# Optimization experiments

Measured on AMD Instinct MI355X. Metric: run time of the kernel, lower is better.

Reference implementation:

```python
import jax, jax.numpy as jnp
import numpy as np

N, H = 8192, 1024

def setup_inputs() -> dict:
    key = jax.random.key(0)
    ks = jax.random.split(key, 7)
    s = 1.0 / np.sqrt(H)
    return {
        "x": jax.random.normal(ks[0], (N, H), dtype=jnp.float32),
        "Wq": jax.random.uniform(ks[1], (H, H), dtype=jnp.float32, minval=-s, maxval=s),
        "bq": jax.random.uniform(ks[2], (H,), dtype=jnp.float32, minval=-s, maxval=s),
        "Wk": jax.random.uniform(ks[3], (H, H), dtype=jnp.float32, minval=-s, maxval=s),
        "bk": jax.random.uniform(ks[4], (H,), dtype=jnp.float32, minval=-s, maxval=s),
        "Wv": jax.random.uniform(ks[5], (H, H), dtype=jnp.float32, minval=-s, maxval=s),
        "bv": jax.random.uniform(ks[6], (H,), dtype=jnp.float32, minval=-s, maxval=s),
    }

def reference(x, Wq, bq, Wk, bk, Wv, bv):
    # q/k/v projections: [N, H]
    q = x @ Wq + bq
    k = x @ Wk + bk
    v = x @ Wv + bv
    # full scores [N, N]; NOTE: original has no 1/sqrt(d) scaling
    scores = q @ k.T
    alpha = jax.nn.softmax(scores, axis=1)
    return alpha @ v
```

## Files before the change

kernel.cpp:

```cpp
#include <hip/hip_runtime.h>
#include <hip/hip_bf16.h>
#include <hip/hip_fp16.h>


typedef _Float16 f16x8 __attribute__((ext_vector_type(8)));
typedef float floatx4 __attribute__((ext_vector_type(4)));

__device__ __forceinline__ unsigned short f2h(float f) {
  __half h = __float2half(f);
  return __builtin_bit_cast(unsigned short, h);
}

__device__ __forceinline__ void async16(const void* g, void* l) {
  __builtin_amdgcn_global_load_lds(
      (__attribute__((address_space(1))) unsigned int*)(g),
      (__attribute__((address_space(3))) unsigned int*)(l),
      16, 0, 0);
}


__global__ __launch_bounds__(256) void conv_f32_f16(const float* __restrict__ in,
                                                    unsigned short* __restrict__ out,
                                                    long n) {
  long i = ((long)blockIdx.x * 256 + threadIdx.x) * 4;
  if (i + 3 < n) {
    float4 f = *(const float4*)(in + i);
    ushort4 o;
    o.x = f2h(f.x); o.y = f2h(f.y); o.z = f2h(f.z); o.w = f2h(f.w);
    *(ushort4*)(out + i) = o;
  }
}

__global__ __launch_bounds__(256) void transpose_f32_f16(const float* __restrict__ in,
                                                         unsigned short* __restrict__ out,
                                                         int rows, int cols) {
  __shared__ float tile[32][33];
  int bx = blockIdx.x * 32;
  int by = blockIdx.y * 32;
  int tx = threadIdx.x & 31, ty = threadIdx.x >> 5;
  #pragma unroll
  for (int yy = ty; yy < 32; yy += 8)
    tile[yy][tx] = in[(size_t)(by + yy) * cols + bx + tx];
  __syncthreads();
  #pragma unroll
  for (int yy = ty; yy < 32; yy += 8)
    out[(size_t)(bx + yy) * rows + by + tx] = f2h(tile[tx][yy]);
}

__global__ __launch_bounds__(256) void transpose_u16(const unsigned short* __restrict__ in,
                                                     unsigned short* __restrict__ out,
                                                     int rows, int cols) {
  __shared__ unsigned short tile[32][33];
  int bx = blockIdx.x * 32;
  int by = blockIdx.y * 32;
  int tx = threadIdx.x & 31, ty = threadIdx.x >> 5;
  #pragma unroll
  for (int yy = ty; yy < 32; yy += 8)
    tile[yy][tx] = in[(size_t)(by + yy) * cols + bx + tx];
  __syncthreads();
  #pragma unroll
  for (int yy = ty; yy < 32; yy += 8)
    out[(size_t)(bx + yy) * rows + by + tx] = tile[tx][yy];
}

template <int MODE>
__global__ __launch_bounds__(256, 2)
void gemm_bt(const unsigned short* __restrict__ A,
             const unsigned short* __restrict__ B,
             int M, int Nn, int K,
             const float* __restrict__ bias,
             void* __restrict__ out) {
  __shared__ unsigned short As[128 * 32];
  __shared__ unsigned short Bs[128 * 32];
  const int tid  = threadIdx.x;
  const int wave = tid >> 6;
  const int lane = tid & 63;
  const int wm = wave >> 1, wn = wave & 1;
  const int quad = lane >> 4, l16 = lane & 15;
  const long bm = (long)blockIdx.y * 128;
  const long bn = (long)blockIdx.x * 128;

  floatx4 acc[4][4] = {};

  const int srow = wave * 32 + (lane >> 2);
  const int scol = (lane & 3) * 8;
  const unsigned short* gA0 = A + (bm + srow) * (long)K + scol;
  const unsigned short* gA1 = gA0 + 16L * K;
  const unsigned short* gB0 = B + (bn + srow) * (long)K + scol;
  const unsigned short* gB1 = gB0 + 16L * K;
  unsigned short* lA0 = &As[(wave * 32) * 32];
  unsigned short* lA1 = &As[(wave * 32 + 16) * 32];
  unsigned short* lB0 = &Bs[(wave * 32) * 32];
  unsigned short* lB1 = &Bs[(wave * 32 + 16) * 32];

  for (int kk = 0; kk < K; kk += 32) {
    async16(gA0 + kk, lA0);
    async16(gA1 + kk, lA1);
    async16(gB0 + kk, lB0);
    async16(gB1 + kk, lB1);
    __syncthreads();
    f16x8 af[4], bfv[4];
    #pragma unroll
    for (int i = 0; i < 4; ++i) {
      af[i]  = *reinterpret_cast<const f16x8*>(&As[(wm * 64 + i * 16 + l16) * 32 + quad * 8]);
      bfv[i] = *reinterpret_cast<const f16x8*>(&Bs[(wn * 64 + i * 16 + l16) * 32 + quad * 8]);
    }
    #pragma unroll
    for (int i = 0; i < 4; ++i)
      #pragma unroll
      for (int j = 0; j < 4; ++j)
        acc[i][j] = __builtin_amdgcn_mfma_f32_16x16x32_f16(af[i], bfv[j], acc[i][j], 0, 0, 0);
    __syncthreads();
  }

  #pragma unroll
  for (int i = 0; i < 4; ++i) {
    const long row0 = bm + wm * 64 + i * 16 + quad * 4;
    #pragma unroll
    for (int j = 0; j < 4; ++j) {
      const long col = bn + wn * 64 + j * 16 + l16;
      float badd = 0.0f;
      if constexpr (MODE == 0) badd = bias[col];
      #pragma unroll
      for (int r = 0; r < 4; ++r) {
        const float v = acc[i][j][r] + badd;
        const long idx = (row0 + r) * (long)Nn + col;
        if constexpr (MODE == 0) {
          ((unsigned short*)out)[idx] = f2h(v);
        } else if constexpr (MODE == 1) {
          ((unsigned short*)out)[idx] = f2h(v);
        } else {
          ((float*)out)[idx] = v;
        }
      }
    }
  }
}

__global__ __launch_bounds__(256) void softmax_rows(unsigned short* __restrict__ S, int n) {
  const int row = blockIdx.x;
  const int tid = threadIdx.x;
  const int lane = tid & 63, w = tid >> 6;
  unsigned short* prow = S + (size_t)row * n;
  const __half* hrow = (const __half*)prow;

  float v[32];
  float m = -1e30f;
  #pragma unroll
  for (int i = 0; i < 32; ++i) {
    v[i] = __half2float(hrow[i * 256 + tid]);
    m = fmaxf(m, v[i]);
  }
  #pragma unroll
  for (int off = 32; off > 0; off >>= 1) m = fmaxf(m, __shfl_down(m, off, 64));
  __shared__ float redm[4];
  if (lane == 0) redm[w] = m;
  __syncthreads();
  m = fmaxf(fmaxf(redm[0], redm[1]), fmaxf(redm[2], redm[3]));

  float s = 0.0f;
  #pragma unroll
  for (int i = 0; i < 32; ++i) {
    v[i] = __expf(v[i] - m);
    s += v[i];
  }
  #pragma unroll
  for (int off = 32; off > 0; off >>= 1) s += __shfl_down(s, off, 64);
  __shared__ float reds[4];
  if (lane == 0) reds[w] = s;
  __syncthreads();
  s = reds[0] + reds[1] + reds[2] + reds[3];
  const float inv = 1.0f / s;

  #pragma unroll
  for (int i = 0; i < 32; ++i) prow[i * 256 + tid] = f2h(v[i] * inv);
}

extern "C" void kernel_launch(void* const* d_in, const int* in_sizes, int n_in,
                              void* d_out, int out_size, void* d_ws, size_t ws_size,
                              hipStream_t stream) {
  const int N = 8192, H = 1024;
  const float* x  = (const float*)d_in[0];
  const float* Wq = (const float*)d_in[1];
  const float* bq = (const float*)d_in[2];
  const float* Wk = (const float*)d_in[3];
  const float* bk = (const float*)d_in[4];
  const float* Wv = (const float*)d_in[5];
  const float* bv = (const float*)d_in[6];

  char* p = (char*)d_ws;
  unsigned short* xh  = (unsigned short*)p; p += (size_t)N * H * 2;
  unsigned short* WqT = (unsigned short*)p; p += (size_t)H * H * 2;
  unsigned short* WkT = (unsigned short*)p; p += (size_t)H * H * 2;
  unsigned short* WvT = (unsigned short*)p; p += (size_t)H * H * 2;
  unsigned short* qh  = (unsigned short*)p; p += (size_t)N * H * 2;
  unsigned short* kh  = (unsigned short*)p; p += (size_t)N * H * 2;
  unsigned short* vh  = (unsigned short*)p; p += (size_t)N * H * 2;
  unsigned short* vth = (unsigned short*)p; p += (size_t)N * H * 2;
  unsigned short* S   = (unsigned short*)p; p += (size_t)N * N * 2;
  if ((size_t)(p - (char*)d_ws) > ws_size) return;

  conv_f32_f16<<<(N * H / 4 + 255) / 256, 256, 0, stream>>>(x, xh, (long)N * H);
  transpose_f32_f16<<<dim3(H / 32, H / 32), 256, 0, stream>>>(Wq, WqT, H, H);
  transpose_f32_f16<<<dim3(H / 32, H / 32), 256, 0, stream>>>(Wk, WkT, H, H);
  transpose_f32_f16<<<dim3(H / 32, H / 32), 256, 0, stream>>>(Wv, WvT, H, H);

  gemm_bt<0><<<dim3(H / 128, N / 128), 256, 0, stream>>>(xh, WqT, N, H, H, bq, qh);
  gemm_bt<0><<<dim3(H / 128, N / 128), 256, 0, stream>>>(xh, WkT, N, H, H, bk, kh);
  gemm_bt<0><<<dim3(H / 128, N / 128), 256, 0, stream>>>(xh, WvT, N, H, H, bv, vh);
  transpose_u16<<<dim3(H / 32, N / 32), 256, 0, stream>>>(vh, vth, N, H);

  gemm_bt<1><<<dim3(N / 128, N / 128), 256, 0, stream>>>(qh, kh, N, N, H, nullptr, S);
  softmax_rows<<<N, 256, 0, stream>>>(S, N);
  gemm_bt<2><<<dim3(H / 128, N / 128), 256, 0, stream>>>(S, vth, N, H, N, nullptr, d_out);
}
```

Baseline: 636.8 us.

## Batch QKV projections, raise GEMM occupancy, split-K PV GEMM with atomics

Merges the three weight transposes and three QKV projection GEMMs into single launches indexed by blockIdx.z. It raises the occupancy hint on gemm_bt from 2 to 4 blocks per SM. The final P·V GEMM is replaced by a 512-thread kernel with a 128x256 tile and a 2-way split over K, accumulating into a zeroed fp32 output with atomicAdd. This cuts launch overhead and gives more blocks to the PV stage, at the cost of a memset, atomic traffic and possible register pressure under the tighter launch bound.

Measured after the change: 601.8 us. -5.5%, faster.

```diff
diff --git a/kernel.cpp b/kernel.cpp
--- a/kernel.cpp
+++ b/kernel.cpp
@@ -31,9 +31,13 @@
   }
 }
 
-__global__ __launch_bounds__(256) void transpose_f32_f16(const float* __restrict__ in,
-                                                         unsigned short* __restrict__ out,
-                                                         int rows, int cols) {
+__global__ __launch_bounds__(256) void transpose_f32_f16_3(const float* __restrict__ in0,
+                                                           const float* __restrict__ in1,
+                                                           const float* __restrict__ in2,
+                                                           unsigned short* __restrict__ out,
+                                                           int rows, int cols) {
+  const float* in = (blockIdx.z == 0) ? in0 : (blockIdx.z == 1) ? in1 : in2;
+  unsigned short* o = out + (size_t)blockIdx.z * rows * cols;
   __shared__ float tile[32][33];
   int bx = blockIdx.x * 32;
   int by = blockIdx.y * 32;
@@ -44,7 +48,7 @@
   __syncthreads();
   #pragma unroll
   for (int yy = ty; yy < 32; yy += 8)
-    out[(size_t)(bx + yy) * rows + by + tx] = f2h(tile[tx][yy]);
+    o[(size_t)(bx + yy) * rows + by + tx] = f2h(tile[tx][yy]);
 }
 
 __global__ __launch_bounds__(256) void transpose_u16(const unsigned short* __restrict__ in,
@@ -64,12 +68,19 @@
 }
 
 template <int MODE>
-__global__ __launch_bounds__(256, 2)
+__global__ __launch_bounds__(256, 4)
 void gemm_bt(const unsigned short* __restrict__ A,
              const unsigned short* __restrict__ B,
              int M, int Nn, int K,
-             const float* __restrict__ bias,
-             void* __restrict__ out) {
+             const float* __restrict__ b0, const float* __restrict__ b1,
+             const float* __restrict__ b2,
+             unsigned short* __restrict__ out) {
+  if constexpr (MODE == 0) {
+    B   += (size_t)blockIdx.z * Nn * K;
+    out += (size_t)blockIdx.z * M * Nn;
+  }
+  const float* bias = (MODE != 0) ? nullptr
+                      : (blockIdx.z == 0) ? b0 : (blockIdx.z == 1) ? b1 : b2;
   __shared__ unsigned short As[128 * 32];
   __shared__ unsigned short Bs[128 * 32];
   const int tid  = threadIdx.x;
@@ -119,20 +130,69 @@
     #pragma unroll
     for (int j = 0; j < 4; ++j) {
       const long col = bn + wn * 64 + j * 16 + l16;
-      float badd = 0.0f;
-      if constexpr (MODE == 0) badd = bias[col];
-      #pragma unroll
-      for (int r = 0; r < 4; ++r) {
-        const float v = acc[i][j][r] + badd;
-        const long idx = (row0 + r) * (long)Nn + col;
-        if constexpr (MODE == 0) {
-          ((unsigned short*)out)[idx] = f2h(v);
-        } else if constexpr (MODE == 1) {
-          ((unsigned short*)out)[idx] = f2h(v);
-        } else {
-          ((float*)out)[idx] = v;
-        }
-      }
+      float badd = (MODE == 0) ? bias[col] : 0.0f;
+      #pragma unroll
+      for (int r = 0; r < 4; ++r)
+        out[(row0 + r) * (long)Nn + col] = f2h(acc[i][j][r] + badd);
+    }
+  }
+}
+
+__global__ __launch_bounds__(512, 4)
+void gemm_pv(const unsigned short* __restrict__ A,
+             const unsigned short* __restrict__ B,
+             int M, int Nn, int K, int kchunk,
+             float* __restrict__ out) {
+  __shared__ unsigned short As[128 * 32];
+  __shared__ unsigned short Bs[256 * 32];
+  const int tid  = threadIdx.x;
+  const int wave = tid >> 6;
+  const int lane = tid & 63;
+  const int wm = wave >> 2;
+  const int wn = wave & 3;
+  const int quad = lane >> 4, l16 = lane & 15;
+  const long bm = (long)blockIdx.y * 128;
+  const long bn = (long)blockIdx.x * 256;
+  const int kbase = blockIdx.z * kchunk;
+
+  floatx4 acc[4][4] = {};
+
+  const int scol = (lane & 3) * 8;
+  const unsigned short* gA  = A + (bm + wave * 16 + (lane >> 2)) * (long)K + scol + kbase;
+  const unsigned short* gB0 = B + (bn + wave * 32 + (lane >> 2)) * (long)K + scol + kbase;
+  const unsigned short* gB1 = gB0 + 16L * K;
+  unsigned short* lA  = &As[(wave * 16) * 32];
+  unsigned short* lB0 = &Bs[(wave * 32) * 32];
+  unsigned short* lB1 = &Bs[(wave * 32 + 16) * 32];
+
+  for (int kk = 0; kk < kchunk; kk += 32) {
+    async16(gA + kk, lA);
+    async16(gB0 + kk, lB0);
+    async16(gB1 + kk, lB1);
+    __syncthreads();
+    f16x8 af[4], bfv[4];
+    #pragma unroll
+    for (int i = 0; i < 4; ++i) {
+      af[i]  = *reinterpret_cast<const f16x8*>(&As[(wm * 64 + i * 16 + l16) * 32 + quad * 8]);
+      bfv[i] = *reinterpret_cast<const f16x8*>(&Bs[(wn * 64 + i * 16 + l16) * 32 + quad * 8]);
+    }
+    #pragma unroll
+    for (int i = 0; i < 4; ++i)
+      #pragma unroll
+      for (int j = 0; j < 4; ++j)
+        acc[i][j] = __builtin_amdgcn_mfma_f32_16x16x32_f16(af[i], bfv[j], acc[i][j], 0, 0, 0);
+    __syncthreads();
+  }
+
+  #pragma unroll
+  for (int i = 0; i < 4; ++i) {
+    const long row0 = bm + wm * 64 + i * 16 + quad * 4;
+    #pragma unroll
+    for (int j = 0; j < 4; ++j) {
+      const long col = bn + wn * 64 + j * 16 + l16;
+      #pragma unroll
+      for (int r = 0; r < 4; ++r)
+        atomicAdd(&out[(row0 + r) * (long)Nn + col], acc[i][j][r]);
     }
   }
 }
@@ -190,27 +250,26 @@
 
   char* p = (char*)d_ws;
   unsigned short* xh  = (unsigned short*)p; p += (size_t)N * H * 2;
-  unsigned short* WqT = (unsigned short*)p; p += (size_t)H * H * 2;
-  unsigned short* WkT = (unsigned short*)p; p += (size_t)H * H * 2;
-  unsigned short* WvT = (unsigned short*)p; p += (size_t)H * H * 2;
-  unsigned short* qh  = (unsigned short*)p; p += (size_t)N * H * 2;
-  unsigned short* kh  = (unsigned short*)p; p += (size_t)N * H * 2;
-  unsigned short* vh  = (unsigned short*)p; p += (size_t)N * H * 2;
+  unsigned short* WT  = (unsigned short*)p; p += (size_t)3 * H * H * 2;
+  unsigned short* qkv = (unsigned short*)p; p += (size_t)3 * N * H * 2;
   unsigned short* vth = (unsigned short*)p; p += (size_t)N * H * 2;
   unsigned short* S   = (unsigned short*)p; p += (size_t)N * N * 2;
   if ((size_t)(p - (char*)d_ws) > ws_size) return;
+  unsigned short* qh = qkv;
+  unsigned short* kh = qkv + (size_t)N * H;
+  unsigned short* vh = qkv + (size_t)2 * N * H;
 
   conv_f32_f16<<<(N * H / 4 + 255) / 256, 256, 0, stream>>>(x, xh, (long)N * H);
-  transpose_f32_f16<<<dim3(H / 32, H / 32), 256, 0, stream>>>(Wq, WqT, H, H);
-  transpose_f32_f16<<<dim3(H / 32, H / 32), 256, 0, stream>>>(Wk, WkT, H, H);
-  transpose_f32_f16<<<dim3(H / 32, H / 32), 256, 0, stream>>>(Wv, WvT, H, H);
-
-  gemm_bt<0><<<dim3(H / 128, N / 128), 256, 0, stream>>>(xh, WqT, N, H, H, bq, qh);
-  gemm_bt<0><<<dim3(H / 128, N / 128), 256, 0, stream>>>(xh, WkT, N, H, H, bk, kh);
-  gemm_bt<0><<<dim3(H / 128, N / 128), 256, 0, stream>>>(xh, WvT, N, H, H, bv, vh);
+  transpose_f32_f16_3<<<dim3(H / 32, H / 32, 3), 256, 0, stream>>>(Wq, Wk, Wv, WT, H, H);
+
+  gemm_bt<0><<<dim3(H / 128, N / 128, 3), 256, 0, stream>>>(xh, WT, N, H, H, bq, bk, bv, qkv);
   transpose_u16<<<dim3(H / 32, N / 32), 256, 0, stream>>>(vh, vth, N, H);
 
-  gemm_bt<1><<<dim3(N / 128, N / 128), 256, 0, stream>>>(qh, kh, N, N, H, nullptr, S);
+  gemm_bt<1><<<dim3(N / 128, N / 128), 256, 0, stream>>>(qh, kh, N, N, H,
+                                                         nullptr, nullptr, nullptr, S);
   softmax_rows<<<N, 256, 0, stream>>>(S, N);
-  gemm_bt<2><<<dim3(H / 128, N / 128), 256, 0, stream>>>(S, vth, N, H, N, nullptr, d_out);
-}
+
+  hipMemsetAsync(d_out, 0, (size_t)N * H * 4, stream);
+  gemm_pv<<<dim3(H / 256, N / 128, 2), 512, 0, stream>>>(S, vth, N, H, N, N / 2,
+                                                         (float*)d_out);
+}
```
